# Kernel optimization log

Measured on AMD Instinct MI355X. Metric: run time of the kernel, lower is better.

The kernel has to match this reference:

```python
import jax, jax.numpy as jnp
import numpy as np

B = 256          # batch of molecules
N_ATOM = 1024    # atoms per molecule
N_EDGE = 8192    # directed edges per molecule (avg degree 8)
NEG_SLOPE = 0.01 # torch LeakyReLU default


def setup_inputs() -> dict:
    key = jax.random.key(0)
    ks = jax.random.split(key, 8)
    x = jax.random.normal(ks[0], (B, 3 * N_ATOM), dtype=jnp.float32)
    edge_index = jax.random.randint(ks[1], (2, N_EDGE), 0, N_ATOM, dtype=jnp.int64)
    # GCNConv weights (Glorot-ish small scale) and biases
    W1 = jax.random.normal(ks[2], (3, 64), dtype=jnp.float32) * 0.3
    b1 = jnp.zeros((64,), jnp.float32)
    W2 = jax.random.normal(ks[3], (64, 64), dtype=jnp.float32) * 0.1
    b2 = jnp.zeros((64,), jnp.float32)
    # project MLP: Linear(64,128) + LeakyReLU
    Wp = jax.random.normal(ks[4], (64, 128), dtype=jnp.float32) * 0.1
    bp = jnp.zeros((128,), jnp.float32)
    return {"x": x, "edge_index": edge_index, "W1": W1, "b1": b1,
            "W2": W2, "b2": b2, "Wp": Wp, "bp": bp}


def _leaky_relu(v):
    return jnp.where(v >= 0, v, NEG_SLOPE * v)


def reference(x, edge_index, W1, b1, W2, b2, Wp, bp):
    # x: [B, 3*n_atom] -> node features [B, n_atom, 3]
    bsz, n_feat = x.shape
    n = n_feat // 3
    h = x.reshape(bsz, n, 3)

    src = edge_index[0]  # message sources
    dst = edge_index[1]  # aggregation targets

    # GCN normalization with self-loops: deg[i] = 1 + in-degree(i)
    ones_e = jnp.ones((src.shape[0],), x.dtype)
    deg = jax.ops.segment_sum(ones_e, dst, num_segments=n) + 1.0
    dinv = jax.lax.rsqrt(deg)                # deg^{-1/2}, deg >= 1
    norm_e = dinv[src] * dinv[dst]           # [E]
    norm_self = dinv * dinv                  # self-loop weight per node

    def gcn(h, W, b):
        hw = h @ W                                        # [B, n, d_out]
        msg = hw[:, src, :] * norm_e[None, :, None]       # [B, E, d_out]
        agg = jax.vmap(lambda m: jax.ops.segment_sum(m, dst, num_segments=n))(msg)
        return agg + norm_self[None, :, None] * hw + b

    h = _leaky_relu(gcn(h, W1, b1))
    h = _leaky_relu(gcn(h, W2, b2))

    # global_mean_pool: every graph has exactly n atoms -> mean over atom axis
    g = h.mean(axis=1)                                    # [B, 64]

    # project MLP: Linear + LeakyReLU
    return _leaky_relu(g @ Wp + bp)                       # [B, 128]
```

## Files before the change

kernel.cpp:

```cpp
#include <hip/hip_runtime.h>

#define N_ATOMS 1024
#define N_EDGES 8192
#define EPAD    (N_EDGES + N_ATOMS)
#define NBATCH  256
#define NEG     0.01f

typedef unsigned int u32;
typedef __attribute__((ext_vector_type(2))) float f32x2;
typedef __attribute__((ext_vector_type(4))) float f32x4;
typedef __attribute__((ext_vector_type(8))) short bf16x8;

__device__ __forceinline__ u32 cvtpk(float lo, float hi) {
    u32 r;
    asm("v_cvt_pk_bf16_f32 %0, %1, %2" : "=v"(r) : "v"(lo), "v"(hi));
    return r;
}
__device__ __forceinline__ f32x2 bfpair(u32 u) {
    f32x2 h;
    h.x = __uint_as_float(u << 16);
    h.y = __uint_as_float(u & 0xffff0000u);
    return h;
}

#define ROWPTR_OFF 0
#define COLW_OFF   4352
#define SELFW_OFF  (4352 + 73728)
#define PERM_OFF   (SELFW_OFF + 4096)
#define W2T_OFF    (PERM_OFF + 4096)

#define TSTR_B 144
#define SM_TILE_BYTES (N_ATOMS * TSTR_B)
#define SM_CT_OFF SM_TILE_BYTES
#define SM_TOTAL (SM_TILE_BYTES + 12288)

__global__ __launch_bounds__(1024) void build_csr(
    const int* __restrict__ ei,
    int*  __restrict__ rowptr,
    int2* __restrict__ colw,
    float* __restrict__ selfw_g,
    int*  __restrict__ perm_g,
    u32*  __restrict__ w2t,
    const float* __restrict__ W2)
{
    __shared__ int   sdeg[N_ATOMS];
    __shared__ int   sstart[N_ATOMS];
    __shared__ float sdinv[N_ATOMS];
    __shared__ int   wtot[16];
    __shared__ int   hist[128];
    const int t = threadIdx.x;
    const int lane = t & 63;
    const int w = t >> 6;
    const int* srcA = ei;
    const int* dstA = ei + N_EDGES;

    sdeg[t] = 0;
    if (t < 128) hist[t] = 0;
    for (int e = t; e < EPAD; e += 1024) colw[e] = make_int2(0, 0);
    __syncthreads();
    for (int e = t; e < N_EDGES; e += 1024) atomicAdd(&sdeg[dstA[e]], 1);
    __syncthreads();

    const int deg  = sdeg[t];
    const int pdeg = (deg + 1) & ~1;
    int v = pdeg;
    #pragma unroll
    for (int d = 1; d < 64; d <<= 1) {
        int u = __shfl_up(v, d, 64);
        if (lane >= d) v += u;
    }
    if (lane == 63) wtot[w] = v;
    __syncthreads();
    if (t == 0) {
        int run = 0;
        #pragma unroll
        for (int i = 0; i < 16; ++i) { int c = wtot[i]; wtot[i] = run; run += c; }
    }
    __syncthreads();
    const int start = v - pdeg + wtot[w];
    sstart[t] = start;
    const float dv = rsqrtf((float)deg + 1.0f);
    sdinv[t] = dv;
    rowptr[t] = start;
    if (t == N_ATOMS - 1) rowptr[N_ATOMS] = start + pdeg;
    selfw_g[t] = dv * dv;

    #pragma unroll
    for (int i = 0; i < 2; ++i) {
        const int idx = t + i * 1024;
        const int c = idx >> 5, kk = idx & 31;
        w2t[c * 32 + kk] = cvtpk(W2[(2 * kk) * 64 + c], W2[(2 * kk + 1) * 64 + c]);
    }

    const int dcl = deg < 127 ? deg : 127;
    atomicAdd(&hist[dcl], 1);
    sdeg[t] = 0;
    __syncthreads();
    if (t == 0) {
        int run = 0;
        for (int i = 0; i < 128; ++i) { int c = hist[i]; hist[i] = run; run += c; }
    }
    __syncthreads();
    const int pos = atomicAdd(&hist[dcl], 1);
    perm_g[pos] = t;
    __syncthreads();

    for (int e = t; e < N_EDGES; e += 1024) {
        const int d = dstA[e];
        const int s = srcA[e];
        const int slot = atomicAdd(&sdeg[d], 1);
        const float wgt = sdinv[s] * sdinv[d];
        colw[sstart[d] + slot] = make_int2(s, __float_as_int(wgt));
    }
}

__global__ __launch_bounds__(1024, 4) void gnn_main(
    const float* __restrict__ x,
    const int*  __restrict__ rowptr,
    const int2* __restrict__ colw,
    const float* __restrict__ selfw_g,
    const int*  __restrict__ perm_g,
    const float* __restrict__ W1, const float* __restrict__ b1,
    const u32*  __restrict__ w2t, const float* __restrict__ b2,
    const float* __restrict__ Wp, const float* __restrict__ bp,
    float* __restrict__ out)
{
    extern __shared__ char smem[];
    float* ctile = (float*)(smem + SM_CT_OFF);
    float* wpool = ctile;
    float* gvec  = ctile + 1024;
    float* proj  = ctile + 1152;

    const int t = threadIdx.x;
    const int b = blockIdx.x;
    const float* xb = x + (size_t)b * (3 * N_ATOMS);

    const int atom = perm_g[t];
    const int s0 = rowptr[atom], s1 = rowptr[atom + 1];
    const float sw = selfw_g[atom];

    #pragma unroll
    for (int i = 0; i < 3; ++i) ctile[t + i * 1024] = xb[t + i * 1024];
    __syncthreads();

    u32 pw[32];
    {
        const float* crs = ctile + atom * 3;
        float A0 = sw * crs[0], A1 = sw * crs[1], A2 = sw * crs[2];
        for (int j = s0; j < s1; j += 2) {
            const int4 cw = *(const int4*)(colw + j);
            const float* c0 = ctile + cw.x * 3;
            const float* c1 = ctile + cw.z * 3;
            const float w0 = __int_as_float(cw.y), w1 = __int_as_float(cw.w);
            A0 += w0 * c0[0] + w1 * c1[0];
            A1 += w0 * c0[1] + w1 * c1[1];
            A2 += w0 * c0[2] + w1 * c1[2];
        }
        #pragma unroll
        for (int p = 0; p < 32; ++p) {
            f32x2 vv = *(const f32x2*)(b1 + 2 * p);
            vv = __builtin_elementwise_fma((f32x2){A0, A0}, *(const f32x2*)(W1 + 2 * p), vv);
            vv = __builtin_elementwise_fma((f32x2){A1, A1}, *(const f32x2*)(W1 + 64 + 2 * p), vv);
            vv = __builtin_elementwise_fma((f32x2){A2, A2}, *(const f32x2*)(W1 + 128 + 2 * p), vv);
            vv.x = fmaxf(vv.x, NEG * vv.x);
            vv.y = fmaxf(vv.y, NEG * vv.y);
            pw[p] = cvtpk(vv.x, vv.y);
        }
        uint4* trow = (uint4*)(smem + (size_t)atom * TSTR_B);
        #pragma unroll
        for (int q = 0; q < 8; ++q)
            trow[q] = make_uint4(pw[4 * q], pw[4 * q + 1], pw[4 * q + 2], pw[4 * q + 3]);
    }
    __syncthreads();

    f32x2 acc[32];
    {
        const f32x2 sw2 = {sw, sw};
        #pragma unroll
        for (int p = 0; p < 32; ++p) acc[p] = bfpair(pw[p]) * sw2;
        for (int j = s0; j < s1; j += 2) {
            const int4 cw = *(const int4*)(colw + j);
            const uint4* rA = (const uint4*)(smem + (size_t)cw.x * TSTR_B);
            const uint4* rB = (const uint4*)(smem + (size_t)cw.z * TSTR_B);
            const f32x2 wA = {__int_as_float(cw.y), __int_as_float(cw.y)};
            const f32x2 wB = {__int_as_float(cw.w), __int_as_float(cw.w)};
            #pragma unroll
            for (int m = 0; m < 8; ++m) {
                const uint4 qA = rA[m];
                acc[4*m+0] = __builtin_elementwise_fma(bfpair(qA.x), wA, acc[4*m+0]);
                acc[4*m+1] = __builtin_elementwise_fma(bfpair(qA.y), wA, acc[4*m+1]);
                acc[4*m+2] = __builtin_elementwise_fma(bfpair(qA.z), wA, acc[4*m+2]);
                acc[4*m+3] = __builtin_elementwise_fma(bfpair(qA.w), wA, acc[4*m+3]);
                const uint4 qB = rB[m];
                acc[4*m+0] = __builtin_elementwise_fma(bfpair(qB.x), wB, acc[4*m+0]);
                acc[4*m+1] = __builtin_elementwise_fma(bfpair(qB.y), wB, acc[4*m+1]);
                acc[4*m+2] = __builtin_elementwise_fma(bfpair(qB.z), wB, acc[4*m+2]);
                acc[4*m+3] = __builtin_elementwise_fma(bfpair(qB.w), wB, acc[4*m+3]);
            }
        }
    }
    __syncthreads();

    {
        u32 pb[32];
        #pragma unroll
        for (int p = 0; p < 32; ++p) pb[p] = cvtpk(acc[p].x, acc[p].y);
        uint4* trow = (uint4*)(smem + (size_t)atom * TSTR_B);
        #pragma unroll
        for (int q = 0; q < 8; ++q)
            trow[q] = make_uint4(pb[4 * q], pb[4 * q + 1], pb[4 * q + 2], pb[4 * q + 3]);
    }

    {
        const int l15 = t & 15;
        const int lq  = (t & 63) >> 4;
        const int w   = t >> 6;

        bf16x8 wf[2][4];
        #pragma unroll
        for (int kt = 0; kt < 2; ++kt)
            #pragma unroll
            for (int ct = 0; ct < 4; ++ct)
                wf[kt][ct] = *(const bf16x8*)(w2t + (ct * 16 + l15) * 32 + kt * 16 + lq * 4);
        float bias[4];
        #pragma unroll
        for (int ct = 0; ct < 4; ++ct) bias[ct] = b2[ct * 16 + l15];

        float pool[4] = {0.f, 0.f, 0.f, 0.f};
        #pragma unroll
        for (int rt = 0; rt < 4; ++rt) {
            const int arow = __shfl(atom, rt * 16 + l15, 64);
            const char* ab = smem + (size_t)arow * TSTR_B + lq * 16;
            const bf16x8 a0 = *(const bf16x8*)(ab);
            const bf16x8 a1 = *(const bf16x8*)(ab + 64);
            #pragma unroll
            for (int ct = 0; ct < 4; ++ct) {
                f32x4 cf = {0.f, 0.f, 0.f, 0.f};
                cf = __builtin_amdgcn_mfma_f32_16x16x32_bf16(a0, wf[0][ct], cf, 0, 0, 0);
                cf = __builtin_amdgcn_mfma_f32_16x16x32_bf16(a1, wf[1][ct], cf, 0, 0, 0);
                float s = 0.0f;
                #pragma unroll
                for (int r = 0; r < 4; ++r) {
                    const float vv = cf[r] + bias[ct];
                    s += fmaxf(vv, NEG * vv);
                }
                pool[ct] += s;
            }
        }
        #pragma unroll
        for (int ct = 0; ct < 4; ++ct) {
            pool[ct] += __shfl_xor(pool[ct], 16, 64);
            pool[ct] += __shfl_xor(pool[ct], 32, 64);
        }
        if ((t & 63) < 16) {
            #pragma unroll
            for (int ct = 0; ct < 4; ++ct)
                wpool[w * 64 + ct * 16 + l15] = pool[ct];
        }
    }
    __syncthreads();

    if (t < 64) {
        float s = 0.0f;
        #pragma unroll
        for (int w = 0; w < 16; ++w) s += wpool[w * 64 + t];
        gvec[t] = s * (1.0f / 1024.0f);
    }
    __syncthreads();
    if (t < 512) {
        const int col = t & 127, pc = t >> 7;
        float s = 0.0f;
        #pragma unroll
        for (int f = 0; f < 16; ++f)
            s += gvec[pc * 16 + f] * Wp[(pc * 16 + f) * 128 + col];
        proj[pc * 128 + col] = s;
    }
    __syncthreads();
    if (t < 128) {
        float s = bp[t] + proj[t] + proj[128 + t] + proj[256 + t] + proj[384 + t];
        s = fmaxf(s, NEG * s);
        out[(size_t)b * 128 + t] = s;
    }
}

extern "C" void kernel_launch(void* const* d_in, const int* in_sizes, int n_in,
                              void* d_out, int out_size, void* d_ws, size_t ws_size,
                              hipStream_t stream) {
    const float* x  = (const float*)d_in[0];
    const int*   ei = (const int*)  d_in[1];
    const float* W1 = (const float*)d_in[2];
    const float* b1 = (const float*)d_in[3];
    const float* W2 = (const float*)d_in[4];
    const float* b2 = (const float*)d_in[5];
    const float* Wp = (const float*)d_in[6];
    const float* bp = (const float*)d_in[7];
    float* out = (float*)d_out;

    char* ws = (char*)d_ws;
    int*   rowptr = (int*)  (ws + ROWPTR_OFF);
    int2*  colw   = (int2*) (ws + COLW_OFF);
    float* selfw  = (float*)(ws + SELFW_OFF);
    int*   perm   = (int*)  (ws + PERM_OFF);
    u32*   w2t    = (u32*)  (ws + W2T_OFF);

    build_csr<<<1, 1024, 0, stream>>>(ei, rowptr, colw, selfw, perm, w2t, W2);

    (void)hipFuncSetAttribute((const void*)gnn_main,
                              hipFuncAttributeMaxDynamicSharedMemorySize, SM_TOTAL);
    gnn_main<<<NBATCH, 1024, SM_TOTAL, stream>>>(
        x, rowptr, colw, selfw, perm, W1, b1, w2t, b2, Wp, bp, out);
}
```

Before: 40.89 us.

## Switch intermediate storage to fp16 with fma_mix and prefetch edge entries

```diff
diff --git a/kernel.cpp b/kernel.cpp
--- a/kernel.cpp
+++ b/kernel.cpp
@@ -9,19 +9,17 @@
 typedef unsigned int u32;
 typedef __attribute__((ext_vector_type(2))) float f32x2;
 typedef __attribute__((ext_vector_type(4))) float f32x4;
-typedef __attribute__((ext_vector_type(8))) short bf16x8;
-
-__device__ __forceinline__ u32 cvtpk(float lo, float hi) {
+typedef __attribute__((ext_vector_type(8))) _Float16 f16x8;
+
+__device__ __forceinline__ u32 pkrtz(float lo, float hi) {
     u32 r;
-    asm("v_cvt_pk_bf16_f32 %0, %1, %2" : "=v"(r) : "v"(lo), "v"(hi));
+    asm("v_cvt_pkrtz_f16_f32 %0, %1, %2" : "=v"(r) : "v"(lo), "v"(hi));
     return r;
 }
-__device__ __forceinline__ f32x2 bfpair(u32 u) {
-    f32x2 h;
-    h.x = __uint_as_float(u << 16);
-    h.y = __uint_as_float(u & 0xffff0000u);
-    return h;
-}
+#define FMIX_LO(a, w, u) \
+    asm("v_fma_mix_f32 %0, %1, %2, %0 op_sel_hi:[0,1,0]" : "+v"(a) : "v"(w), "v"(u))
+#define FMIX_HI(a, w, u) \
+    asm("v_fma_mix_f32 %0, %1, %2, %0 op_sel:[0,1,0] op_sel_hi:[0,1,0]" : "+v"(a) : "v"(w), "v"(u))
 
 #define ROWPTR_OFF 0
 #define COLW_OFF   4352
@@ -32,7 +30,7 @@
 #define TSTR_B 144
 #define SM_TILE_BYTES (N_ATOMS * TSTR_B)
 #define SM_CT_OFF SM_TILE_BYTES
-#define SM_TOTAL (SM_TILE_BYTES + 12288)
+#define SM_TOTAL (SM_TILE_BYTES + 16384)
 
 __global__ __launch_bounds__(1024) void build_csr(
     const int* __restrict__ ei,
@@ -89,7 +87,7 @@
     for (int i = 0; i < 2; ++i) {
         const int idx = t + i * 1024;
         const int c = idx >> 5, kk = idx & 31;
-        w2t[c * 32 + kk] = cvtpk(W2[(2 * kk) * 64 + c], W2[(2 * kk + 1) * 64 + c]);
+        w2t[c * 32 + kk] = pkrtz(W2[(2 * kk) * 64 + c], W2[(2 * kk + 1) * 64 + c]);
     }
 
     const int dcl = deg < 127 ? deg : 127;
@@ -126,10 +124,11 @@
     float* __restrict__ out)
 {
     extern __shared__ char smem[];
-    float* ctile = (float*)(smem + SM_CT_OFF);
-    float* wpool = ctile;
-    float* gvec  = ctile + 1024;
-    float* proj  = ctile + 1152;
+    float4* ctile4 = (float4*)(smem + SM_CT_OFF);
+    float*  paux   = (float*)ctile4;
+    float*  wpool  = paux;
+    float*  gvec   = paux + 1024;
+    float*  proj   = paux + 1088;
 
     const int t = threadIdx.x;
     const int b = blockIdx.x;
@@ -139,22 +138,29 @@
     const int s0 = rowptr[atom], s1 = rowptr[atom + 1];
     const float sw = selfw_g[atom];
 
-    #pragma unroll
-    for (int i = 0; i < 3; ++i) ctile[t + i * 1024] = xb[t + i * 1024];
+    {
+        float4 c;
+        c.x = xb[3 * t]; c.y = xb[3 * t + 1]; c.z = xb[3 * t + 2]; c.w = 0.0f;
+        ctile4[t] = c;
+    }
     __syncthreads();
 
     u32 pw[32];
     {
-        const float* crs = ctile + atom * 3;
-        float A0 = sw * crs[0], A1 = sw * crs[1], A2 = sw * crs[2];
+        const float4 cs = ctile4[atom];
+        float A0 = sw * cs.x, A1 = sw * cs.y, A2 = sw * cs.z;
+        int4 cur = make_int4(0, 0, 0, 0);
+        if (s0 < s1) cur = *(const int4*)(colw + s0);
         for (int j = s0; j < s1; j += 2) {
-            const int4 cw = *(const int4*)(colw + j);
-            const float* c0 = ctile + cw.x * 3;
-            const float* c1 = ctile + cw.z * 3;
-            const float w0 = __int_as_float(cw.y), w1 = __int_as_float(cw.w);
-            A0 += w0 * c0[0] + w1 * c1[0];
-            A1 += w0 * c0[1] + w1 * c1[1];
-            A2 += w0 * c0[2] + w1 * c1[2];
+            const int jn = (j + 2 < s1) ? (j + 2) : s0;
+            const int4 nxt = *(const int4*)(colw + jn);
+            const float4 c0 = ctile4[cur.x];
+            const float4 c1 = ctile4[cur.z];
+            const float w0 = __int_as_float(cur.y), w1 = __int_as_float(cur.w);
+            A0 += w0 * c0.x + w1 * c1.x;
+            A1 += w0 * c0.y + w1 * c1.y;
+            A2 += w0 * c0.z + w1 * c1.z;
+            cur = nxt;
         }
         #pragma unroll
         for (int p = 0; p < 32; ++p) {
@@ -164,7 +170,7 @@
             vv = __builtin_elementwise_fma((f32x2){A2, A2}, *(const f32x2*)(W1 + 128 + 2 * p), vv);
             vv.x = fmaxf(vv.x, NEG * vv.x);
             vv.y = fmaxf(vv.y, NEG * vv.y);
-            pw[p] = cvtpk(vv.x, vv.y);
+            pw[p] = pkrtz(vv.x, vv.y);
         }
         uint4* trow = (uint4*)(smem + (size_t)atom * TSTR_B);
         #pragma unroll
@@ -173,30 +179,41 @@
     }
     __syncthreads();
 
-    f32x2 acc[32];
-    {
-        const f32x2 sw2 = {sw, sw};
-        #pragma unroll
-        for (int p = 0; p < 32; ++p) acc[p] = bfpair(pw[p]) * sw2;
+    float acc[64];
+    {
+        #pragma unroll
+        for (int f = 0; f < 64; ++f) acc[f] = 0.0f;
+        #pragma unroll
+        for (int p = 0; p < 32; ++p) {
+            FMIX_LO(acc[2 * p],     sw, pw[p]);
+            FMIX_HI(acc[2 * p + 1], sw, pw[p]);
+        }
+        int4 cur = make_int4(0, 0, 0, 0);
+        if (s0 < s1) cur = *(const int4*)(colw + s0);
         for (int j = s0; j < s1; j += 2) {
-            const int4 cw = *(const int4*)(colw + j);
-            const uint4* rA = (const uint4*)(smem + (size_t)cw.x * TSTR_B);
-            const uint4* rB = (const uint4*)(smem + (size_t)cw.z * TSTR_B);
-            const f32x2 wA = {__int_as_float(cw.y), __int_as_float(cw.y)};
-            const f32x2 wB = {__int_as_float(cw.w), __int_as_float(cw.w)};
+            const int jn = (j + 2 < s1) ? (j + 2) : s0;
+            const int4 nxt = *(const int4*)(colw + jn);
+            const uint4* rA = (const uint4*)(smem + (size_t)cur.x * TSTR_B);
+            const uint4* rB = (const uint4*)(smem + (size_t)cur.z * TSTR_B);
+            const float wA = __int_as_float(cur.y);
+            const float wB = __int_as_float(cur.w);
             #pragma unroll
             for (int m = 0; m < 8; ++m) {
                 const uint4 qA = rA[m];
-                acc[4*m+0] = __builtin_elementwise_fma(bfpair(qA.x), wA, acc[4*m+0]);
-                acc[4*m+1] = __builtin_elementwise_fma(bfpair(qA.y), wA, acc[4*m+1]);
-                acc[4*m+2] = __builtin_elementwise_fma(bfpair(qA.z), wA, acc[4*m+2]);
-                acc[4*m+3] = __builtin_elementwise_fma(bfpair(qA.w), wA, acc[4*m+3]);
+                FMIX_LO(acc[8*m+0], wA, qA.x); FMIX_HI(acc[8*m+1], wA, qA.x);
+                FMIX_LO(acc[8*m+2], wA, qA.y); FMIX_HI(acc[8*m+3], wA, qA.y);
+                FMIX_LO(acc[8*m+4], wA, qA.z); FMIX_HI(acc[8*m+5], wA, qA.z);
+                FMIX_LO(acc[8*m+6], wA, qA.w); FMIX_HI(acc[8*m+7], wA, qA.w);
+            }
+            #pragma unroll
+            for (int m = 0; m < 8; ++m) {
                 const uint4 qB = rB[m];
-                acc[4*m+0] = __builtin_elementwise_fma(bfpair(qB.x), wB, acc[4*m+0]);
-                acc[4*m+1] = __builtin_elementwise_fma(bfpair(qB.y), wB, acc[4*m+1]);
-                acc[4*m+2] = __builtin_elementwise_fma(bfpair(qB.z), wB, acc[4*m+2]);
-                acc[4*m+3] = __builtin_elementwise_fma(bfpair(qB.w), wB, acc[4*m+3]);
+                FMIX_LO(acc[8*m+0], wB, qB.x); FMIX_HI(acc[8*m+1], wB, qB.x);
+                FMIX_LO(acc[8*m+2], wB, qB.y); FMIX_HI(acc[8*m+3], wB, qB.y);
+                FMIX_LO(acc[8*m+4], wB, qB.z); FMIX_HI(acc[8*m+5], wB, qB.z);
+                FMIX_LO(acc[8*m+6], wB, qB.w); FMIX_HI(acc[8*m+7], wB, qB.w);
             }
+            cur = nxt;
         }
     }
     __syncthreads();
@@ -204,7 +221,7 @@
     {
         u32 pb[32];
         #pragma unroll
-        for (int p = 0; p < 32; ++p) pb[p] = cvtpk(acc[p].x, acc[p].y);
+        for (int p = 0; p < 32; ++p) pb[p] = pkrtz(acc[2 * p], acc[2 * p + 1]);
         uint4* trow = (uint4*)(smem + (size_t)atom * TSTR_B);
         #pragma unroll
         for (int q = 0; q < 8; ++q)
@@ -216,12 +233,12 @@
         const int lq  = (t & 63) >> 4;
         const int w   = t >> 6;
 
-        bf16x8 wf[2][4];
+        f16x8 wf[2][4];
         #pragma unroll
         for (int kt = 0; kt < 2; ++kt)
             #pragma unroll
             for (int ct = 0; ct < 4; ++ct)
-                wf[kt][ct] = *(const bf16x8*)(w2t + (ct * 16 + l15) * 32 + kt * 16 + lq * 4);
+                wf[kt][ct] = *(const f16x8*)(w2t + (ct * 16 + l15) * 32 + kt * 16 + lq * 4);
         float bias[4];
         #pragma unroll
         for (int ct = 0; ct < 4; ++ct) bias[ct] = b2[ct * 16 + l15];
@@ -231,13 +248,13 @@
         for (int rt = 0; rt < 4; ++rt) {
             const int arow = __shfl(atom, rt * 16 + l15, 64);
             const char* ab = smem + (size_t)arow * TSTR_B + lq * 16;
-            const bf16x8 a0 = *(const bf16x8*)(ab);
-            const bf16x8 a1 = *(const bf16x8*)(ab + 64);
+            const f16x8 a0 = *(const f16x8*)(ab);
+            const f16x8 a1 = *(const f16x8*)(ab + 64);
             #pragma unroll
             for (int ct = 0; ct < 4; ++ct) {
                 f32x4 cf = {0.f, 0.f, 0.f, 0.f};
-                cf = __builtin_amdgcn_mfma_f32_16x16x32_bf16(a0, wf[0][ct], cf, 0, 0, 0);
-                cf = __builtin_amdgcn_mfma_f32_16x16x32_bf16(a1, wf[1][ct], cf, 0, 0, 0);
+                cf = __builtin_amdgcn_mfma_f32_16x16x32_f16(a0, wf[0][ct], cf, 0, 0, 0);
+                cf = __builtin_amdgcn_mfma_f32_16x16x32_f16(a1, wf[1][ct], cf, 0, 0, 0);
                 float s = 0.0f;
                 #pragma unroll
                 for (int r = 0; r < 4; ++r) {
```

New measurement: 39.28 us. 1.04x faster.
